# Optimization experiments

Hardware: AMD Instinct MI355X
Metric: run time of the kernel (lower is better)

The kernel has to match this reference:

```python
import jax, jax.numpy as jnp
import numpy as np

B, T, H, OUT_LEN, D_IN, D_OUT = 512, 512, 256, 8, 64, 64

def _lstm_seq(x, Wih, Whh, bih, bhh):
    # batch_first LSTM, zero initial state; x: [B,T,D] -> [B,T,H]
    b = bih + bhh
    h0 = jnp.zeros((x.shape[0], Whh.shape[1]), x.dtype)
    def step(carry, xt):
        h, c = carry
        g = xt @ Wih.T + h @ Whh.T + b
        i, f, gg, o = jnp.split(g, 4, axis=-1)  # torch gate order i,f,g,o
        c = jax.nn.sigmoid(f) * c + jax.nn.sigmoid(i) * jnp.tanh(gg)
        h = jax.nn.sigmoid(o) * jnp.tanh(c)
        return (h, c), h
    _, hs = jax.lax.scan(step, (h0, h0), jnp.swapaxes(x, 0, 1))
    return jnp.swapaxes(hs, 0, 1)

def _lstm_cell0(xt, Wih, bih, bhh):
    # single decode step; original calls self.dec with fresh zero (h,c) each
    # step, so the recurrent matrix Whh never contributes.
    g = xt @ Wih.T + bih + bhh
    i, f, gg, o = jnp.split(g, 4, axis=-1)
    c = jax.nn.sigmoid(i) * jnp.tanh(gg)
    return jax.nn.sigmoid(o) * jnp.tanh(c)

def _mlp(x, Ws, bs, Wl, bl):
    # simple.mlp: hidden Linear+ReLU stack, linear output (dropout off)
    for k in range(Ws.shape[0]):
        x = jax.nn.relu(x @ Ws[k] + bs[k])
    return x @ Wl + bl

def setup_inputs():
    key = jax.random.key(0)
    ks = iter(jax.random.split(key, 32))
    def W(shape, fan):
        return jax.random.normal(next(ks), shape, jnp.float32) / np.float32(np.sqrt(fan))
    return {
        'x': jax.random.normal(next(ks), (B, T, D_IN), jnp.float32),
        'in_W': W((D_IN, H), D_IN), 'in_b': jnp.zeros((H,), jnp.float32),
        'enc_Wih': W((4*H, H), H), 'enc_Whh': W((4*H, H), H),
        'enc_bih': jnp.zeros((4*H,), jnp.float32), 'enc_bhh': jnp.zeros((4*H,), jnp.float32),
        'dec_Wih': W((4*H, 2*H), 2*H), 'dec_Whh': W((4*H, H), H),
        'dec_bih': jnp.zeros((4*H,), jnp.float32), 'dec_bhh': jnp.zeros((4*H,), jnp.float32),
        'w_Ws': W((3, H, H), H), 'w_bs': jnp.zeros((3, H), jnp.float32), 'w_Wl': W((H, H), H), 'w_bl': jnp.zeros((H,), jnp.float32),
        'u_Ws': W((3, H, H), H), 'u_bs': jnp.zeros((3, H), jnp.float32), 'u_Wl': W((H, H), H), 'u_bl': jnp.zeros((H,), jnp.float32),
        'v_Ws': W((7, H, H), H), 'v_bs': jnp.zeros((7, H), jnp.float32), 'v_Wl': W((H, 1), H), 'v_bl': jnp.zeros((1,), jnp.float32),
        'out_W': W((H, D_OUT), H), 'out_b': jnp.zeros((D_OUT,), jnp.float32),
    }

def reference(x, in_W, in_b, enc_Wih, enc_Whh, enc_bih, enc_bhh,
              dec_Wih, dec_Whh, dec_bih, dec_bhh,
              w_Ws, w_bs, w_Wl, w_bl, u_Ws, u_bs, u_Wl, u_bl,
              v_Ws, v_bs, v_Wl, v_bl, out_W, out_b):
    h = x @ in_W + in_b                                       # input projection [B,T,H]
    enc = _lstm_seq(h, enc_Wih, enc_Whh, enc_bih, enc_bhh)    # [B,T,H]
    whs = _mlp(enc, w_Ws, w_bs, w_Wl, w_bl)                   # w(hs), loop-invariant (hoisted)
    def dec_step(s, _):
        us = _mlp(s, u_Ws, u_bs, u_Wl, u_bl)                  # [B,H]
        e = _mlp(jnp.tanh(us[:, None, :] + whs), v_Ws, v_bs, v_Wl, v_bl)  # [B,T,1]
        a = jax.nn.softmax(e, axis=1)                         # softmax over time
        c_t = jnp.sum(a * enc, axis=1)                        # [B,H] weighted sum
        s_new = _lstm_cell0(jnp.concatenate([c_t, s], axis=-1), dec_Wih, dec_bih, dec_bhh)
        return s_new, s_new
    s0 = jnp.zeros((x.shape[0], H), x.dtype)
    _, ss = jax.lax.scan(dec_step, s0, None, length=OUT_LEN)  # [OUT_LEN,B,H]
    dec = jnp.swapaxes(ss, 0, 1)                              # [B,OUT_LEN,H]
    return dec @ out_W + out_b                                # output projection
```

## Files before the change

### kernel.cpp

```cpp
#include <hip/hip_runtime.h>
#include <math.h>

#define B_    512
#define T_    512
#define H_    256
#define DIN_  64
#define OL_   8
#define DOUT_ 64

typedef unsigned short u16;
typedef unsigned int u32;
typedef unsigned long long ull;
typedef __attribute__((ext_vector_type(8))) short short8;
typedef __attribute__((ext_vector_type(4))) float f32x4;

static __device__ __forceinline__ float sigm(float x){ return 1.0f/(1.0f + expf(-x)); }
static __device__ __forceinline__ float bf2f(u16 h){
  u32 u = ((u32)h) << 16; float f; __builtin_memcpy(&f, &u, 4); return f;
}
static __device__ __forceinline__ u16 f2bf(float f){
  u32 u; __builtin_memcpy(&u, &f, 4);
  u = (u + 0x7fffu + ((u >> 16) & 1u)) >> 16;
  return (u16)u;
}
static __device__ __forceinline__ u32 packhl(float f){
  u16 h = f2bf(f);
  u16 lo = f2bf(f - bf2f(h));
  return ((u32)h << 16) | (u32)lo;
}
static __device__ __forceinline__ float unpackhl(u32 w){
  return bf2f((u16)(w >> 16)) + bf2f((u16)(w & 0xffff));
}

__global__ void k_wpt(const float* __restrict__ inW, const float* __restrict__ Wih,
                      float* __restrict__ WpT)
{
  int gid = blockIdx.x * 256 + threadIdx.x;
  int c = gid >> 6, d = gid & 63;
  const float* wr = Wih + c * H_;
  const float* ir = inW + d * H_;
  float acc = 0.f;
  #pragma unroll 4
  for (int e = 0; e < H_; e += 4) {
    float4 av = *(const float4*)(ir + e);
    float4 bv = *(const float4*)(wr + e);
    acc += av.x*bv.x + av.y*bv.y + av.z*bv.z + av.w*bv.w;
  }
  WpT[c*64 + d] = acc;
}

__global__ void k_bp(const float* __restrict__ inb, const float* __restrict__ Wih,
                     const float* __restrict__ bih, const float* __restrict__ bhh,
                     float* __restrict__ bp)
{
  int c = blockIdx.x * 256 + threadIdx.x;
  const float* wr = Wih + c * H_;
  float acc = bih[c] + bhh[c];
  for (int e = 0; e < H_; ++e) acc += inb[e] * wr[e];
  bp[c] = acc;
}

__global__ void k_dwt(const float* __restrict__ dWih, float* __restrict__ dWt)
{
  int gid = blockIdx.x * 256 + threadIdx.x;
  int j = gid >> 9, k = gid & 511;
  int row = (j < 256) ? j : (j + 256);
  dWt[k*768 + j] = dWih[row*512 + k];
}

__global__ void k_wall(const float* __restrict__ wWs, const float* __restrict__ wWl,
                       const float* __restrict__ uWs, const float* __restrict__ uWl,
                       const float* __restrict__ vWs, u16* __restrict__ outb)
{
  int lyr = blockIdx.y;
  const float* W = (lyr < 3)  ? wWs + lyr*65536
                 : (lyr == 3) ? wWl
                 : (lyr < 7)  ? uWs + (lyr-4)*65536
                 : (lyr == 7) ? uWl
                 :              vWs + (lyr-8)*65536;
  u16* out = outb + (size_t)lyr*131072;
  int gid = blockIdx.x * 256 + threadIdx.x;
  int k = gid & 255, n = gid >> 8;
  float v = W[k*256 + n];
  int s = k >> 5, j = k & 7;
  int lane = (((k >> 3) & 3) << 4) | (n & 15);
  int fl = ((s*16) + (n >> 4))*512 + lane*8 + j;
  u16 h = f2bf(v);
  out[fl] = h;
  out[65536 + fl] = f2bf(v - bf2f(h));
}

__global__ void k_whhfl(const float* __restrict__ Whh, u16* __restrict__ out)
{
  int gid = blockIdx.x * 256 + threadIdx.x;
  int j = gid & 7, l = (gid >> 3) & 63, ctg = (gid >> 9) & 63, s = gid >> 15;
  int k = s*32 + (l >> 4)*8 + j;
  int wv = ctg >> 2, g = ctg & 3;
  int row = g*256 + wv*16 + (l & 15);
  float v = Whh[row*256 + k];
  int fl = (s*64 + ctg)*512 + l*8 + j;
  u16 h = f2bf(v);
  out[fl] = h;
  out[262144 + fl] = f2bf(v - bf2f(h));
}

__global__ void k_wpfl(const float* __restrict__ WpT, u16* __restrict__ out)
{
  int gid = blockIdx.x * 256 + threadIdx.x;
  int j = gid & 7, l = (gid >> 3) & 63, ctg = (gid >> 9) & 63, s = gid >> 15;
  int k = s*32 + (l >> 4)*8 + j;
  int wv = ctg >> 2, g = ctg & 3;
  int row = g*256 + wv*16 + (l & 15);
  float v = WpT[row*64 + k];
  int fl = (s*64 + ctg)*512 + l*8 + j;
  u16 h = f2bf(v);
  out[fl] = h;
  out[65536 + fl] = f2bf(v - bf2f(h));
}

__global__ __launch_bounds__(256,1) void k_enc(
    const float* __restrict__ x, const u16* __restrict__ whhFL,
    const u16* __restrict__ wpFL, const float* __restrict__ bp,
    u32* __restrict__ henc, int CB)
{
  __shared__ float G[2][16][32][4];
  const int tid = threadIdx.x, l = tid & 63, wv = tid >> 6;
  const int lr = l & 15, lk = l >> 4;
  const int rg = blockIdx.x, bg = blockIdx.y, z = blockIdx.z;
  const int ug2 = wv >> 1;
  const int g0 = (wv & 1) * 2;
  const int u16g = bg*2 + ug2;

  short8 whH[8][2], whL[8][2], wpH[2][2], wpL[2][2];
  #pragma unroll
  for (int s = 0; s < 8; ++s)
    #pragma unroll
    for (int c = 0; c < 2; ++c) {
      int ctg = u16g*4 + g0 + c;
      whH[s][c] = *(const short8*)(whhFL + ((size_t)(s*64 + ctg))*512 + l*8);
      whL[s][c] = *(const short8*)(whhFL + 262144 + ((size_t)(s*64 + ctg))*512 + l*8);
    }
  #pragma unroll
  for (int s = 0; s < 2; ++s)
    #pragma unroll
    for (int c = 0; c < 2; ++c) {
      int ctg = u16g*4 + g0 + c;
      wpH[s][c] = *(const short8*)(wpFL + ((size_t)(s*64 + ctg))*512 + l*8);
      wpL[s][c] = *(const short8*)(wpFL + 65536 + ((size_t)(s*64 + ctg))*512 + l*8);
    }
  const int ul = tid & 31, er0 = tid >> 5;
  float bb[4];
  #pragma unroll
  for (int g = 0; g < 4; ++g) bb[g] = bp[g*256 + bg*32 + ul];
  float cs[2] = {0.f, 0.f};

  const size_t hstride = (size_t)CB * 256;
  u32* hz = henc + (size_t)z * (size_t)(T_+1) * hstride;
  const float* xrow = x + ((size_t)(z*CB + rg*16 + lr)*T_)*DIN_ + lk*8;

  for (int t = 0; t < T_; ++t) {
    float4 xv0 = *(const float4*)(xrow);
    float4 xv1 = *(const float4*)(xrow + 4);
    float4 xv2 = *(const float4*)(xrow + 32);
    float4 xv3 = *(const float4*)(xrow + 36);
    xrow += DIN_;

    const ull* hb = (const ull*)(hz + (size_t)t*hstride + (size_t)(rg*16 + lr)*256);
    ull hq[8][4];
    #pragma unroll
    for (int s = 0; s < 8; ++s)
      #pragma unroll
      for (int q = 0; q < 4; ++q)
        hq[s][q] = __hip_atomic_load(hb + s*16 + lk*4 + q,
                                     __ATOMIC_RELAXED, __HIP_MEMORY_SCOPE_AGENT);
    if (t) {
      for (;;) {
        bool ok = true;
        #pragma unroll
        for (int s = 0; s < 8; ++s)
          #pragma unroll
          for (int q = 0; q < 4; ++q) {
            u32 a = (u32)hq[s][q], b = (u32)(hq[s][q] >> 32);
            ok = ok && (a != 0u) && (b != 0u);
          }
        if (__all(ok)) break;
        __builtin_amdgcn_s_sleep(1);
        #pragma unroll
        for (int s = 0; s < 8; ++s)
          #pragma unroll
          for (int q = 0; q < 4; ++q)
            hq[s][q] = __hip_atomic_load(hb + s*16 + lk*4 + q,
                                         __ATOMIC_RELAXED, __HIP_MEMORY_SCOPE_AGENT);
      }
    }

    f32x4 acc[2];
    acc[0] = (f32x4){0.f,0.f,0.f,0.f};
    acc[1] = (f32x4){0.f,0.f,0.f,0.f};

    #pragma unroll
    for (int s = 0; s < 2; ++s) {
      float vv[8];
      if (s == 0) { vv[0]=xv0.x;vv[1]=xv0.y;vv[2]=xv0.z;vv[3]=xv0.w;vv[4]=xv1.x;vv[5]=xv1.y;vv[6]=xv1.z;vv[7]=xv1.w; }
      else        { vv[0]=xv2.x;vv[1]=xv2.y;vv[2]=xv2.z;vv[3]=xv2.w;vv[4]=xv3.x;vv[5]=xv3.y;vv[6]=xv3.z;vv[7]=xv3.w; }
      short8 ah, al;
      #pragma unroll
      for (int j = 0; j < 8; ++j) {
        u16 h = f2bf(vv[j]);
        ah[j] = (short)h;
        al[j] = (short)f2bf(vv[j] - bf2f(h));
      }
      #pragma unroll
      for (int c = 0; c < 2; ++c) {
        acc[c] = __builtin_amdgcn_mfma_f32_16x16x32_bf16(ah, wpH[s][c], acc[c], 0,0,0);
        acc[c] = __builtin_amdgcn_mfma_f32_16x16x32_bf16(al, wpH[s][c], acc[c], 0,0,0);
        acc[c] = __builtin_amdgcn_mfma_f32_16x16x32_bf16(ah, wpL[s][c], acc[c], 0,0,0);
      }
    }
    #pragma unroll
    for (int s = 0; s < 8; ++s) {
      short8 ah, al;
      #pragma unroll
      for (int q = 0; q < 4; ++q) {
        u32 w0 = (u32)hq[s][q], w1 = (u32)(hq[s][q] >> 32);
        ah[q*2]   = (short)(w0 >> 16); al[q*2]   = (short)(w0 & 0xffff);
        ah[q*2+1] = (short)(w1 >> 16); al[q*2+1] = (short)(w1 & 0xffff);
      }
      #pragma unroll
      for (int c = 0; c < 2; ++c) {
        acc[c] = __builtin_amdgcn_mfma_f32_16x16x32_bf16(ah, whH[s][c], acc[c], 0,0,0);
        acc[c] = __builtin_amdgcn_mfma_f32_16x16x32_bf16(al, whH[s][c], acc[c], 0,0,0);
        acc[c] = __builtin_amdgcn_mfma_f32_16x16x32_bf16(ah, whL[s][c], acc[c], 0,0,0);
      }
    }

    const int p = t & 1;
    #pragma unroll
    for (int c = 0; c < 2; ++c)
      #pragma unroll
      for (int j = 0; j < 4; ++j)
        G[p][lk*4 + j][ug2*16 + lr][g0 + c] = acc[c][j];
    __syncthreads();

    #pragma unroll
    for (int pp = 0; pp < 2; ++pp) {
      int row = er0 + pp*8;
      float4 gq = *(const float4*)&G[p][row][ul][0];
      float gi = gq.x + bb[0], gf = gq.y + bb[1];
      float gg = gq.z + bb[2], go = gq.w + bb[3];
      float cn = sigm(gf)*cs[pp] + sigm(gi)*tanhf(gg);
      float hn = sigm(go)*tanhf(cn);
      cs[pp] = cn;
      __hip_atomic_store(hz + (size_t)(t+1)*hstride + (size_t)(rg*16 + row)*256 + bg*32 + ul,
                         packhl(hn) | 1u, __ATOMIC_RELAXED, __HIP_MEMORY_SCOPE_AGENT);
    }
  }
}

template<int IN, int FIN, int OUTP>
__global__ __launch_bounds__(256,2) void k_mlp(
    const float* __restrict__ A0, const float* __restrict__ usp,
    const u16* __restrict__ wFL, const float* __restrict__ bs,
    const float* __restrict__ bl, float* __restrict__ Cout,
    float* __restrict__ eout, const float* __restrict__ vWl,
    const float* __restrict__ vbl, int L, int nbs, int cbm1)
{
  extern __shared__ u32 act[];
  const int tid = threadIdx.x, l = tid & 63, cg = tid >> 6;
  const int lr = l & 15, lk = l >> 4;
  const long m0 = (long)blockIdx.x * 64;

  for (int i = tid; i < 4096; i += 256) {
    int row = i >> 6, c16 = i & 63;
    long m = m0 + row;
    uint4 pk;
    if (IN == 2) {
      pk = *(const uint4*)((const u32*)A0 + m*256 + c16*4);
    } else {
      float4 v;
      if (IN == 3) {
        uint4 pw = *(const uint4*)((const u32*)A0 + m*256 + c16*4);
        v.x = unpackhl(pw.x); v.y = unpackhl(pw.y);
        v.z = unpackhl(pw.z); v.w = unpackhl(pw.w);
      } else {
        v = *(const float4*)(A0 + m*256 + c16*4);
      }
      if (IN == 1 || IN == 3) {
        const float* ub = usp + (size_t)(m & cbm1)*256;
        float4 u4 = *(const float4*)(ub + c16*4);
        v.x = tanhf(v.x + u4.x); v.y = tanhf(v.y + u4.y);
        v.z = tanhf(v.z + u4.z); v.w = tanhf(v.w + u4.w);
      }
      pk = (uint4){packhl(v.x), packhl(v.y), packhl(v.z), packhl(v.w)};
    }
    *((uint4*)(act + row*256 + ((c16 ^ (row & 7)) << 2))) = pk;
  }

  f32x4 acc[4][4];
  for (int lyr = 0; lyr < L; ++lyr) {
    __syncthreads();
    const u16* wb = wFL + (size_t)lyr*131072;
    #pragma unroll
    for (int rt = 0; rt < 4; ++rt)
      #pragma unroll
      for (int ct = 0; ct < 4; ++ct) acc[rt][ct] = (f32x4){0.f,0.f,0.f,0.f};

    short8 bh[2][4], blo[2][4];
    #pragma unroll
    for (int ct = 0; ct < 4; ++ct) {
      const u16* bfp = wb + ((size_t)(cg*4 + ct))*512 + l*8;
      bh[0][ct]  = *(const short8*)bfp;
      blo[0][ct] = *(const short8*)(bfp + 65536);
    }
    #pragma unroll
    for (int s = 0; s < 8; ++s) {
      const int pb = s & 1, nb = pb ^ 1;
      if (s < 7) {
        #pragma unroll
        for (int ct = 0; ct < 4; ++ct) {
          const u16* bfp = wb + ((size_t)((s+1)*16 + cg*4 + ct))*512 + l*8;
          bh[nb][ct]  = *(const short8*)bfp;
          blo[nb][ct] = *(const short8*)(bfp + 65536);
        }
      }
      short8 ah[4], al[4];
      #pragma unroll
      for (int rt = 0; rt < 4; ++rt) {
        int row = rt*16 + lr;
        int cc = s*8 + lk*2;
        const u32* base = act + row*256;
        uint4 d0 = *(const uint4*)(base + (((cc    ) ^ (row & 7)) << 2));
        uint4 d1 = *(const uint4*)(base + (((cc + 1) ^ (row & 7)) << 2));
        u32 q[8] = {d0.x,d0.y,d0.z,d0.w,d1.x,d1.y,d1.z,d1.w};
        #pragma unroll
        for (int j = 0; j < 8; ++j) {
          ah[rt][j] = (short)(q[j] >> 16);
          al[rt][j] = (short)(q[j] & 0xffff);
        }
      }
      #pragma unroll
      for (int ct = 0; ct < 4; ++ct)
        #pragma unroll
        for (int rt = 0; rt < 4; ++rt) {
          acc[rt][ct] = __builtin_amdgcn_mfma_f32_16x16x32_bf16(ah[rt], bh[pb][ct],  acc[rt][ct], 0,0,0);
          acc[rt][ct] = __builtin_amdgcn_mfma_f32_16x16x32_bf16(al[rt], bh[pb][ct],  acc[rt][ct], 0,0,0);
          acc[rt][ct] = __builtin_amdgcn_mfma_f32_16x16x32_bf16(ah[rt], blo[pb][ct], acc[rt][ct], 0,0,0);
        }
    }
    const float* bptr = (lyr < nbs) ? (bs + lyr*256) : bl;
    const bool dorelu = (lyr < L-1) || (FIN == 1);
    #pragma unroll
    for (int ct = 0; ct < 4; ++ct) {
      float bv = bptr[cg*64 + ct*16 + lr];
      #pragma unroll
      for (int rt = 0; rt < 4; ++rt)
        #pragma unroll
        for (int g = 0; g < 4; ++g) {
          float xv = acc[rt][ct][g] + bv;
          acc[rt][ct][g] = dorelu ? fmaxf(xv, 0.f) : xv;
        }
    }
    if (lyr == L-1) break;
    __syncthreads();
    #pragma unroll
    for (int ct = 0; ct < 4; ++ct) {
      int n = cg*64 + ct*16 + lr;
      #pragma unroll
      for (int rt = 0; rt < 4; ++rt)
        #pragma unroll
        for (int g = 0; g < 4; ++g) {
          int row = rt*16 + lk*4 + g;
          act[row*256 + (((n >> 2) ^ (row & 7)) << 2) + (n & 3)] = packhl(acc[rt][ct][g]);
        }
    }
  }

  if (FIN == 0) {
    #pragma unroll
    for (int ct = 0; ct < 4; ++ct) {
      int n = cg*64 + ct*16 + lr;
      #pragma unroll
      for (int rt = 0; rt < 4; ++rt)
        #pragma unroll
        for (int g = 0; g < 4; ++g) {
          long m = m0 + rt*16 + lk*4 + g;
          if (OUTP) ((u32*)Cout)[m*256 + n] = packhl(acc[rt][ct][g]);
          else      Cout[m*256 + n] = acc[rt][ct][g];
        }
    }
  } else {
    float part[4][4];
    #pragma unroll
    for (int rt = 0; rt < 4; ++rt)
      #pragma unroll
      for (int g = 0; g < 4; ++g) part[rt][g] = 0.f;
    #pragma unroll
    for (int ct = 0; ct < 4; ++ct) {
      float vw = vWl[cg*64 + ct*16 + lr];
      #pragma unroll
      for (int rt = 0; rt < 4; ++rt)
        #pragma unroll
        for (int g = 0; g < 4; ++g) part[rt][g] += acc[rt][ct][g] * vw;
    }
    #pragma unroll
    for (int o = 1; o < 16; o <<= 1)
      #pragma unroll
      for (int rt = 0; rt < 4; ++rt)
        #pragma unroll
        for (int g = 0; g < 4; ++g) part[rt][g] += __shfl_xor(part[rt][g], o, 64);
    __syncthreads();
    float* ep = (float*)act;
    if ((l & 15) == 0) {
      #pragma unroll
      for (int rt = 0; rt < 4; ++rt)
        #pragma unroll
        for (int g = 0; g < 4; ++g)
          ep[cg*64 + rt*16 + lk*4 + g] = part[rt][g];
    }
    __syncthreads();
    if (tid < 64)
      eout[m0 + tid] = ep[tid] + ep[64 + tid] + ep[128 + tid] + ep[192 + tid] + vbl[0];
  }
}

__global__ __launch_bounds__(256,2) void k_attn(const float* __restrict__ e,
    const u32* __restrict__ henc, float* __restrict__ ct, int CB)
{
  __shared__ float as[512];
  __shared__ float red[8];
  const int b = blockIdx.x, tid = threadIdx.x;
  const int lane = tid & 63, w = tid >> 6;
  float v0 = e[(size_t)tid*CB + b];
  float v1 = e[(size_t)(tid + 256)*CB + b];
  float m = fmaxf(v0, v1);
  #pragma unroll
  for (int o = 32; o; o >>= 1) m = fmaxf(m, __shfl_xor(m, o, 64));
  if (!lane) red[w] = m;
  __syncthreads();
  m = fmaxf(fmaxf(red[0], red[1]), fmaxf(red[2], red[3]));
  float x0 = expf(v0 - m), x1 = expf(v1 - m);
  float sm = x0 + x1;
  #pragma unroll
  for (int o = 32; o; o >>= 1) sm += __shfl_xor(sm, o, 64);
  if (!lane) red[4 + w] = sm;
  __syncthreads();
  float inv = 1.f / (red[4] + red[5] + red[6] + red[7]);
  as[tid] = x0 * inv;
  as[256 + tid] = x1 * inv;
  __syncthreads();
  float acc = 0.f;
  const u32* ep = henc + (size_t)(CB + b)*256 + tid;
  const size_t ts = (size_t)CB * 256;
  #pragma unroll 8
  for (int t = 0; t < 512; ++t) acc += as[t] * unpackhl(ep[t*ts]);
  ct[b*H_ + tid] = acc;
}

__global__ __launch_bounds__(256,2) void k_dec_cell(
    const float* __restrict__ ct, float* __restrict__ s, const float* __restrict__ dWt,
    const float* __restrict__ bih, const float* __restrict__ bhh,
    float* __restrict__ dec, int step)
{
  __shared__ float xt[4][516];
  const int tid = threadIdx.x;
  const int b0 = blockIdx.x * 4;
  for (int f = tid; f < 4*128; f += 256) {
    int bb = f >> 7, k4 = f & 127;
    float4 v = (k4 < 64) ? *(const float4*)(ct + (b0+bb)*H_ + k4*4)
                         : *(const float4*)(s  + (b0+bb)*H_ + (k4-64)*4);
    *(float4*)(&xt[bb][k4*4]) = v;
  }
  __syncthreads();
  const int u = tid;
  float ai[4], ag[4], ao[4];
  #pragma unroll
  for (int bb = 0; bb < 4; ++bb) { ai[bb]=0.f; ag[bb]=0.f; ao[bb]=0.f; }
  #pragma unroll 4
  for (int k = 0; k < 512; ++k) {
    float wi = dWt[k*768 + u];
    float wg = dWt[k*768 + 256 + u];
    float wo = dWt[k*768 + 512 + u];
    #pragma unroll
    for (int bb = 0; bb < 4; ++bb) {
      float xv = xt[bb][k];
      ai[bb] += xv*wi; ag[bb] += xv*wg; ao[bb] += xv*wo;
    }
  }
  float bi = bih[u]       + bhh[u];
  float bg = bih[512 + u] + bhh[512 + u];
  float bo = bih[768 + u] + bhh[768 + u];
  #pragma unroll
  for (int bb = 0; bb < 4; ++bb) {
    int b = b0 + bb;
    float cn = sigm(ai[bb] + bi) * tanhf(ag[bb] + bg);
    float hn = sigm(ao[bb] + bo) * tanhf(cn);
    s[b*H_ + u] = hn;
    dec[((size_t)b*OL_ + step)*H_ + u] = hn;
  }
}

__global__ __launch_bounds__(256,2) void k_outproj(
    const float* __restrict__ dec, const float* __restrict__ oW,
    const float* __restrict__ ob, float* __restrict__ out)
{
  const int tid = threadIdx.x;
  const int m0 = blockIdx.x * 16;
  const int d = tid & 63, rr = tid >> 6;
  float bv = ob[d];
  for (int p = 0; p < 4; ++p) {
    int m = m0 + p*4 + rr;
    const float* ar = dec + (size_t)m*H_;
    float acc = bv;
    #pragma unroll 4
    for (int k = 0; k < H_; ++k) acc += ar[k] * oW[k*64 + d];
    out[(size_t)m*64 + d] = acc;
  }
}

extern "C" void kernel_launch(void* const* d_in, const int* in_sizes, int n_in,
                              void* d_out, int out_size, void* d_ws, size_t ws_size,
                              hipStream_t stream)
{
  (void)in_sizes; (void)n_in;
  const float* x    = (const float*)d_in[0];
  const float* inW  = (const float*)d_in[1];
  const float* inb  = (const float*)d_in[2];
  const float* eWih = (const float*)d_in[3];
  const float* eWhh = (const float*)d_in[4];
  const float* ebih = (const float*)d_in[5];
  const float* ebhh = (const float*)d_in[6];
  const float* dWih = (const float*)d_in[7];
  const float* dbih = (const float*)d_in[9];
  const float* dbhh = (const float*)d_in[10];
  const float* wWs  = (const float*)d_in[11];
  const float* wbs  = (const float*)d_in[12];
  const float* wWl  = (const float*)d_in[13];
  const float* wbl  = (const float*)d_in[14];
  const float* uWs  = (const float*)d_in[15];
  const float* ubs  = (const float*)d_in[16];
  const float* uWl  = (const float*)d_in[17];
  const float* ubl  = (const float*)d_in[18];
  const float* vWs  = (const float*)d_in[19];
  const float* vbs  = (const float*)d_in[20];
  const float* vWl  = (const float*)d_in[21];
  const float* vbl  = (const float*)d_in[22];
  const float* oW   = (const float*)d_in[23];
  const float* ob   = (const float*)d_in[24];
  float* out = (float*)d_out;

  hipFuncSetAttribute((const void*)k_mlp<0,0,0>, hipFuncAttributeMaxDynamicSharedMemorySize, 65536);
  hipFuncSetAttribute((const void*)k_mlp<2,0,1>, hipFuncAttributeMaxDynamicSharedMemorySize, 65536);
  hipFuncSetAttribute((const void*)k_mlp<3,1,0>, hipFuncAttributeMaxDynamicSharedMemorySize, 65536);

  const int CB = 128;
  const size_t hsz = (size_t)(T_+1)*CB*256;
  const size_t avail = ws_size / 4;
  auto need = [&](int nc) -> size_t {
    return (size_t)nc*hsz
         + (size_t)CB*T_*256/1
         - (size_t)CB*T_*256 + (size_t)CB*T_*256
         + (size_t)CB*3328 + 1300000ull;
  };
  auto needf = [&](int nc) -> size_t {
    return (size_t)nc*hsz + (size_t)CB*T_*256 + (size_t)CB*3328 + 1300000ull;
  };
  (void)need;
  int NC = (needf(2) <= avail) ? 2 : 1;
  if (needf(NC) > avail) { hipMemsetAsync(d_out, 0, (size_t)out_size*4, stream); return; }

  float* wsf = (float*)d_ws;
  size_t o = 0;
  u32* henc = (u32*)(wsf + o);  o += (size_t)NC*hsz;
  u32* whsP = (u32*)(wsf + o);  o += (size_t)CB*T_*256;
  float* sbuf= wsf + o;  o += (size_t)CB*256;
  float* us  = wsf + o;  o += (size_t)CB*256;
  float* ctx = wsf + o;  o += (size_t)CB*256;
  float* dec = wsf + o;  o += (size_t)CB*2048;
  float* e   = wsf + o;  o += (size_t)CB*512;
  float* WpT = wsf + o;  o += 65536;
  float* bp  = wsf + o;  o += 1024;
  float* dWt = wsf + o;  o += 393216;
  u16* whhFL = (u16*)(wsf + o);  o += 262144;
  u16* wpFL  = (u16*)(wsf + o);  o += 65536;
  u16* mlpFL = (u16*)(wsf + o);

  k_wpt<<<256, 256, 0, stream>>>(inW, eWih, WpT);
  k_bp <<<4,   256, 0, stream>>>(inb, eWih, ebih, ebhh, bp);
  k_dwt<<<1536,256, 0, stream>>>(dWih, dWt);
  k_whhfl<<<1024,256,0,stream>>>(eWhh, whhFL);
  k_wpfl <<<256, 256,0,stream>>>(WpT, wpFL);
  k_wall <<<dim3(256,15), 256, 0, stream>>>(wWs, wWl, uWs, uWl, vWs, mlpFL);

  const int gBig = CB * 8;
  const int gU   = CB / 64;
  const int cbm1 = CB - 1;

  for (int c0 = 0; c0 < B_; c0 += CB*NC) {
    hipMemsetAsync(henc, 0, (size_t)NC*hsz*4, stream);

    k_enc<<<dim3(CB/16, 8, NC), 256, 0, stream>>>(
        x + (size_t)c0*T_*DIN_, whhFL, wpFL, bp, henc, CB);

    for (int z = 0; z < NC; ++z) {
      int c = c0 + z*CB;
      u32* hz = henc + (size_t)z*hsz;
      float* outc = out + (size_t)c*OL_*DOUT_;

      hipMemsetAsync(sbuf, 0, (size_t)CB*1024, stream);

      k_mlp<2,0,1><<<gBig, 256, 65536, stream>>>((const float*)(hz + (size_t)CB*256),
                                                 nullptr, mlpFL, wbs, wbl,
                                                 (float*)whsP, nullptr, nullptr, nullptr, 4, 3, 0);

      for (int step = 0; step < OL_; ++step) {
        k_mlp<0,0,0><<<gU, 256, 65536, stream>>>(sbuf, nullptr, mlpFL + 4ull*131072, ubs, ubl,
                                                 us, nullptr, nullptr, nullptr, 4, 3, 0);
        k_mlp<3,1,0><<<gBig, 256, 65536, stream>>>((const float*)whsP, us, mlpFL + 8ull*131072,
                                                   vbs, nullptr, nullptr, e, vWl, vbl, 7, 7, cbm1);
        k_attn<<<CB, 256, 0, stream>>>(e, hz, ctx, CB);
        k_dec_cell<<<CB/4, 256, 0, stream>>>(ctx, sbuf, dWt, dbih, dbhh, dec, step);
      }
      k_outproj<<<CB/2, 256, 0, stream>>>(dec, oW, ob, outc);
    }
  }
}
```

Baseline: 19.20 ms.

## Fuse decoder stages into one persistent kernel with flag-based inter-block sync

```diff
diff --git a/kernel.cpp b/kernel.cpp
--- a/kernel.cpp
+++ b/kernel.cpp
@@ -8,6 +8,9 @@
 #define OL_   8
 #define DOUT_ 64
 
+#define CBv   128
+#define HSTR  32768
+
 typedef unsigned short u16;
 typedef unsigned int u32;
 typedef unsigned long long ull;
@@ -30,6 +33,12 @@
 }
 static __device__ __forceinline__ float unpackhl(u32 w){
   return bf2f((u16)(w >> 16)) + bf2f((u16)(w & 0xffff));
+}
+static __device__ __forceinline__ u32 al(const u32* p){
+  return __hip_atomic_load(p, __ATOMIC_RELAXED, __HIP_MEMORY_SCOPE_AGENT);
+}
+static __device__ __forceinline__ void as_(u32* p, u32 v){
+  __hip_atomic_store(p, v, __ATOMIC_RELAXED, __HIP_MEMORY_SCOPE_AGENT);
 }
 
 __global__ void k_wpt(const float* __restrict__ inW, const float* __restrict__ Wih,
@@ -121,7 +130,7 @@
 __global__ __launch_bounds__(256,1) void k_enc(
     const float* __restrict__ x, const u16* __restrict__ whhFL,
     const u16* __restrict__ wpFL, const float* __restrict__ bp,
-    u32* __restrict__ henc, int CB)
+    u32* __restrict__ henc)
 {
   __shared__ float G[2][16][32][4];
   const int tid = threadIdx.x, l = tid & 63, wv = tid >> 6;
@@ -154,9 +163,8 @@
   for (int g = 0; g < 4; ++g) bb[g] = bp[g*256 + bg*32 + ul];
   float cs[2] = {0.f, 0.f};
 
-  const size_t hstride = (size_t)CB * 256;
-  u32* hz = henc + (size_t)z * (size_t)(T_+1) * hstride;
-  const float* xrow = x + ((size_t)(z*CB + rg*16 + lr)*T_)*DIN_ + lk*8;
+  u32* hz = henc + (size_t)z * (size_t)(T_+1) * HSTR;
+  const float* xrow = x + ((size_t)(z*CBv + rg*16 + lr)*T_)*DIN_ + lk*8;
 
   for (int t = 0; t < T_; ++t) {
     float4 xv0 = *(const float4*)(xrow);
@@ -165,7 +173,7 @@
     float4 xv3 = *(const float4*)(xrow + 36);
     xrow += DIN_;
 
-    const ull* hb = (const ull*)(hz + (size_t)t*hstride + (size_t)(rg*16 + lr)*256);
+    const ull* hb = (const ull*)(hz + (size_t)t*HSTR + (size_t)(rg*16 + lr)*256);
     ull hq[8][4];
     #pragma unroll
     for (int s = 0; s < 8; ++s)
@@ -203,34 +211,34 @@
       float vv[8];
       if (s == 0) { vv[0]=xv0.x;vv[1]=xv0.y;vv[2]=xv0.z;vv[3]=xv0.w;vv[4]=xv1.x;vv[5]=xv1.y;vv[6]=xv1.z;vv[7]=xv1.w; }
       else        { vv[0]=xv2.x;vv[1]=xv2.y;vv[2]=xv2.z;vv[3]=xv2.w;vv[4]=xv3.x;vv[5]=xv3.y;vv[6]=xv3.z;vv[7]=xv3.w; }
-      short8 ah, al;
+      short8 ah, al2;
       #pragma unroll
       for (int j = 0; j < 8; ++j) {
         u16 h = f2bf(vv[j]);
         ah[j] = (short)h;
-        al[j] = (short)f2bf(vv[j] - bf2f(h));
+        al2[j] = (short)f2bf(vv[j] - bf2f(h));
       }
       #pragma unroll
       for (int c = 0; c < 2; ++c) {
-        acc[c] = __builtin_amdgcn_mfma_f32_16x16x32_bf16(ah, wpH[s][c], acc[c], 0,0,0);
-        acc[c] = __builtin_amdgcn_mfma_f32_16x16x32_bf16(al, wpH[s][c], acc[c], 0,0,0);
-        acc[c] = __builtin_amdgcn_mfma_f32_16x16x32_bf16(ah, wpL[s][c], acc[c], 0,0,0);
+        acc[c] = __builtin_amdgcn_mfma_f32_16x16x32_bf16(ah,  wpH[s][c], acc[c], 0,0,0);
+        acc[c] = __builtin_amdgcn_mfma_f32_16x16x32_bf16(al2, wpH[s][c], acc[c], 0,0,0);
+        acc[c] = __builtin_amdgcn_mfma_f32_16x16x32_bf16(ah,  wpL[s][c], acc[c], 0,0,0);
       }
     }
     #pragma unroll
     for (int s = 0; s < 8; ++s) {
-      short8 ah, al;
+      short8 ah, al2;
       #pragma unroll
       for (int q = 0; q < 4; ++q) {
         u32 w0 = (u32)hq[s][q], w1 = (u32)(hq[s][q] >> 32);
-        ah[q*2]   = (short)(w0 >> 16); al[q*2]   = (short)(w0 & 0xffff);
-        ah[q*2+1] = (short)(w1 >> 16); al[q*2+1] = (short)(w1 & 0xffff);
+        ah[q*2]   = (short)(w0 >> 16); al2[q*2]   = (short)(w0 & 0xffff);
+        ah[q*2+1] = (short)(w1 >> 16); al2[q*2+1] = (short)(w1 & 0xffff);
       }
       #pragma unroll
       for (int c = 0; c < 2; ++c) {
-        acc[c] = __builtin_amdgcn_mfma_f32_16x16x32_bf16(ah, whH[s][c], acc[c], 0,0,0);
-        acc[c] = __builtin_amdgcn_mfma_f32_16x16x32_bf16(al, whH[s][c], acc[c], 0,0,0);
-        acc[c] = __builtin_amdgcn_mfma_f32_16x16x32_bf16(ah, whL[s][c], acc[c], 0,0,0);
+        acc[c] = __builtin_amdgcn_mfma_f32_16x16x32_bf16(ah,  whH[s][c], acc[c], 0,0,0);
+        acc[c] = __builtin_amdgcn_mfma_f32_16x16x32_bf16(al2, whH[s][c], acc[c], 0,0,0);
+        acc[c] = __builtin_amdgcn_mfma_f32_16x16x32_bf16(ah,  whL[s][c], acc[c], 0,0,0);
       }
     }
 
@@ -251,51 +259,18 @@
       float cn = sigm(gf)*cs[pp] + sigm(gi)*tanhf(gg);
       float hn = sigm(go)*tanhf(cn);
       cs[pp] = cn;
-      __hip_atomic_store(hz + (size_t)(t+1)*hstride + (size_t)(rg*16 + row)*256 + bg*32 + ul,
-                         packhl(hn) | 1u, __ATOMIC_RELAXED, __HIP_MEMORY_SCOPE_AGENT);
+      as_(hz + (size_t)(t+1)*HSTR + (size_t)(rg*16 + row)*256 + bg*32 + ul,
+          packhl(hn) | 1u);
     }
   }
 }
 
-template<int IN, int FIN, int OUTP>
-__global__ __launch_bounds__(256,2) void k_mlp(
-    const float* __restrict__ A0, const float* __restrict__ usp,
-    const u16* __restrict__ wFL, const float* __restrict__ bs,
-    const float* __restrict__ bl, float* __restrict__ Cout,
-    float* __restrict__ eout, const float* __restrict__ vWl,
-    const float* __restrict__ vbl, int L, int nbs, int cbm1)
-{
-  extern __shared__ u32 act[];
-  const int tid = threadIdx.x, l = tid & 63, cg = tid >> 6;
+static __device__ __forceinline__ void mlp_core(
+    u32* act, const u16* wFL, const float* bs, const float* bl,
+    int L, int nbs, bool lastRelu, int tid)
+{
+  const int l = tid & 63, cg = tid >> 6;
   const int lr = l & 15, lk = l >> 4;
-  const long m0 = (long)blockIdx.x * 64;
-
-  for (int i = tid; i < 4096; i += 256) {
-    int row = i >> 6, c16 = i & 63;
-    long m = m0 + row;
-    uint4 pk;
-    if (IN == 2) {
-      pk = *(const uint4*)((const u32*)A0 + m*256 + c16*4);
-    } else {
-      float4 v;
-      if (IN == 3) {
-        uint4 pw = *(const uint4*)((const u32*)A0 + m*256 + c16*4);
-        v.x = unpackhl(pw.x); v.y = unpackhl(pw.y);
-        v.z = unpackhl(pw.z); v.w = unpackhl(pw.w);
-      } else {
-        v = *(const float4*)(A0 + m*256 + c16*4);
-      }
-      if (IN == 1 || IN == 3) {
-        const float* ub = usp + (size_t)(m & cbm1)*256;
-        float4 u4 = *(const float4*)(ub + c16*4);
-        v.x = tanhf(v.x + u4.x); v.y = tanhf(v.y + u4.y);
-        v.z = tanhf(v.z + u4.z); v.w = tanhf(v.w + u4.w);
-      }
-      pk = (uint4){packhl(v.x), packhl(v.y), packhl(v.z), packhl(v.w)};
-    }
-    *((uint4*)(act + row*256 + ((c16 ^ (row & 7)) << 2))) = pk;
-  }
-
   f32x4 acc[4][4];
   for (int lyr = 0; lyr < L; ++lyr) {
     __syncthreads();
@@ -323,7 +298,7 @@
           blo[nb][ct] = *(const short8*)(bfp + 65536);
         }
       }
-      short8 ah[4], al[4];
+      short8 ah[4], al2[4];
       #pragma unroll
       for (int rt = 0; rt < 4; ++rt) {
         int row = rt*16 + lr;
@@ -334,21 +309,21 @@
         u32 q[8] = {d0.x,d0.y,d0.z,d0.w,d1.x,d1.y,d1.z,d1.w};
         #pragma unroll
         for (int j = 0; j < 8; ++j) {
-          ah[rt][j] = (short)(q[j] >> 16);
-          al[rt][j] = (short)(q[j] & 0xffff);
+          ah[rt][j]  = (short)(q[j] >> 16);
+          al2[rt][j] = (short)(q[j] & 0xffff);
         }
       }
       #pragma unroll
       for (int ct = 0; ct < 4; ++ct)
         #pragma unroll
         for (int rt = 0; rt < 4; ++rt) {
-          acc[rt][ct] = __builtin_amdgcn_mfma_f32_16x16x32_bf16(ah[rt], bh[pb][ct],  acc[rt][ct], 0,0,0);
-          acc[rt][ct] = __builtin_amdgcn_mfma_f32_16x16x32_bf16(al[rt], bh[pb][ct],  acc[rt][ct], 0,0,0);
-          acc[rt][ct] = __builtin_amdgcn_mfma_f32_16x16x32_bf16(ah[rt], blo[pb][ct], acc[rt][ct], 0,0,0);
+          acc[rt][ct] = __builtin_amdgcn_mfma_f32_16x16x32_bf16(ah[rt],  bh[pb][ct],  acc[rt][ct], 0,0,0);
+          acc[rt][ct] = __builtin_amdgcn_mfma_f32_16x16x32_bf16(al2[rt], bh[pb][ct],  acc[rt][ct], 0,0,0);
+          acc[rt][ct] = __builtin_amdgcn_mfma_f32_16x16x32_bf16(ah[rt],  blo[pb][ct], acc[rt][ct], 0,0,0);
         }
     }
     const float* bptr = (lyr < nbs) ? (bs + lyr*256) : bl;
-    const bool dorelu = (lyr < L-1) || (FIN == 1);
+    const bool dorelu = (lyr < L-1) || lastRelu;
     #pragma unroll
     for (int ct = 0; ct < 4; ++ct) {
       float bv = bptr[cg*64 + ct*16 + lr];
@@ -360,7 +335,6 @@
           acc[rt][ct][g] = dorelu ? fmaxf(xv, 0.f) : xv;
         }
     }
-    if (lyr == L-1) break;
     __syncthreads();
     #pragma unroll
     for (int ct = 0; ct < 4; ++ct) {
@@ -374,146 +348,216 @@
         }
     }
   }
-
-  if (FIN == 0) {
-    #pragma unroll
-    for (int ct = 0; ct < 4; ++ct) {
-      int n = cg*64 + ct*16 + lr;
-      #pragma unroll
-      for (int rt = 0; rt < 4; ++rt)
-        #pragma unroll
-        for (int g = 0; g < 4; ++g) {
-          long m = m0 + rt*16 + lk*4 + g;
-          if (OUTP) ((u32*)Cout)[m*256 + n] = packhl(acc[rt][ct][g]);
-          else      Cout[m*256 + n] = acc[rt][ct][g];
-        }
-    }
-  } else {
-    float part[4][4];
-    #pragma unroll
-    for (int rt = 0; rt < 4; ++rt)
-      #pragma unroll
-      for (int g = 0; g < 4; ++g) part[rt][g] = 0.f;
-    #pragma unroll
-    for (int ct = 0; ct < 4; ++ct) {
-      float vw = vWl[cg*64 + ct*16 + lr];
-      #pragma unroll
-      for (int rt = 0; rt < 4; ++rt)
-        #pragma unroll
-        for (int g = 0; g < 4; ++g) part[rt][g] += acc[rt][ct][g] * vw;
-    }
-    #pragma unroll
-    for (int o = 1; o < 16; o <<= 1)
-      #pragma unroll
-      for (int rt = 0; rt < 4; ++rt)
-        #pragma unroll
-        for (int g = 0; g < 4; ++g) part[rt][g] += __shfl_xor(part[rt][g], o, 64);
+  __syncthreads();
+}
+
+__global__ __launch_bounds__(256,1) void k_dec_all(
+    const u32* __restrict__ henc, const u16* __restrict__ mlpFL,
+    const float* __restrict__ wbs, const float* __restrict__ wbl,
+    const float* __restrict__ ubs, const float* __restrict__ ubl,
+    const float* __restrict__ vbs, const float* __restrict__ vWl,
+    const float* __restrict__ vbl,
+    const float* __restrict__ dWt, const float* __restrict__ dbih,
+    const float* __restrict__ dbhh,
+    const float* __restrict__ oW, const float* __restrict__ ob,
+    u32* __restrict__ whsP, u32* __restrict__ usb, u32* __restrict__ usflag,
+    u32* __restrict__ eS, u32* __restrict__ ctxS, u32* __restrict__ sS,
+    float* __restrict__ outc)
+{
+  extern __shared__ u32 act[];
+  __shared__ float red[8];
+  const int bid = blockIdx.x, tid = threadIdx.x;
+  const u16* wFLw = mlpFL;
+  const u16* wFLu = mlpFL + 4*131072;
+  const u16* wFLv = mlpFL + 8*131072;
+  float sprev[4] = {0.f, 0.f, 0.f, 0.f};
+
+  for (int k = 0; k < 4; ++k) {
+    long m0t = (long)(bid + 256*k) * 64;
     __syncthreads();
-    float* ep = (float*)act;
-    if ((l & 15) == 0) {
-      #pragma unroll
-      for (int rt = 0; rt < 4; ++rt)
-        #pragma unroll
-        for (int g = 0; g < 4; ++g)
-          ep[cg*64 + rt*16 + lk*4 + g] = part[rt][g];
-    }
-    __syncthreads();
-    if (tid < 64)
-      eout[m0 + tid] = ep[tid] + ep[64 + tid] + ep[128 + tid] + ep[192 + tid] + vbl[0];
+    for (int i = tid; i < 4096; i += 256) {
+      int row = i >> 6, c16 = i & 63;
+      long m = m0t + row;
+      uint4 pk = *(const uint4*)(henc + HSTR + m*256 + c16*4);
+      *((uint4*)(act + row*256 + ((c16 ^ (row & 7)) << 2))) = pk;
+    }
+    mlp_core(act, wFLw, wbs, wbl, 4, 3, false, tid);
+    for (int i = tid; i < 4096; i += 256) {
+      int row = i >> 6, c16 = i & 63;
+      long m = m0t + row;
+      uint4 pk = *((const uint4*)(act + row*256 + ((c16 ^ (row & 7)) << 2)));
+      *(uint4*)(whsP + m*256 + c16*4) = pk;
+    }
   }
-}
-
-__global__ __launch_bounds__(256,2) void k_attn(const float* __restrict__ e,
-    const u32* __restrict__ henc, float* __restrict__ ct, int CB)
-{
-  __shared__ float as[512];
-  __shared__ float red[8];
-  const int b = blockIdx.x, tid = threadIdx.x;
-  const int lane = tid & 63, w = tid >> 6;
-  float v0 = e[(size_t)tid*CB + b];
-  float v1 = e[(size_t)(tid + 256)*CB + b];
-  float m = fmaxf(v0, v1);
-  #pragma unroll
-  for (int o = 32; o; o >>= 1) m = fmaxf(m, __shfl_xor(m, o, 64));
-  if (!lane) red[w] = m;
-  __syncthreads();
-  m = fmaxf(fmaxf(red[0], red[1]), fmaxf(red[2], red[3]));
-  float x0 = expf(v0 - m), x1 = expf(v1 - m);
-  float sm = x0 + x1;
-  #pragma unroll
-  for (int o = 32; o; o >>= 1) sm += __shfl_xor(sm, o, 64);
-  if (!lane) red[4 + w] = sm;
-  __syncthreads();
-  float inv = 1.f / (red[4] + red[5] + red[6] + red[7]);
-  as[tid] = x0 * inv;
-  as[256 + tid] = x1 * inv;
-  __syncthreads();
-  float acc = 0.f;
-  const u32* ep = henc + (size_t)(CB + b)*256 + tid;
-  const size_t ts = (size_t)CB * 256;
-  #pragma unroll 8
-  for (int t = 0; t < 512; ++t) acc += as[t] * unpackhl(ep[t*ts]);
-  ct[b*H_ + tid] = acc;
-}
-
-__global__ __launch_bounds__(256,2) void k_dec_cell(
-    const float* __restrict__ ct, float* __restrict__ s, const float* __restrict__ dWt,
-    const float* __restrict__ bih, const float* __restrict__ bhh,
-    float* __restrict__ dec, int step)
-{
-  __shared__ float xt[4][516];
-  const int tid = threadIdx.x;
-  const int b0 = blockIdx.x * 4;
-  for (int f = tid; f < 4*128; f += 256) {
-    int bb = f >> 7, k4 = f & 127;
-    float4 v = (k4 < 64) ? *(const float4*)(ct + (b0+bb)*H_ + k4*4)
-                         : *(const float4*)(s  + (b0+bb)*H_ + (k4-64)*4);
-    *(float4*)(&xt[bb][k4*4]) = v;
-  }
-  __syncthreads();
-  const int u = tid;
-  float ai[4], ag[4], ao[4];
-  #pragma unroll
-  for (int bb = 0; bb < 4; ++bb) { ai[bb]=0.f; ag[bb]=0.f; ao[bb]=0.f; }
-  #pragma unroll 4
-  for (int k = 0; k < 512; ++k) {
-    float wi = dWt[k*768 + u];
-    float wg = dWt[k*768 + 256 + u];
-    float wo = dWt[k*768 + 512 + u];
-    #pragma unroll
-    for (int bb = 0; bb < 4; ++bb) {
-      float xv = xt[bb][k];
-      ai[bb] += xv*wi; ag[bb] += xv*wg; ao[bb] += xv*wo;
-    }
-  }
-  float bi = bih[u]       + bhh[u];
-  float bg = bih[512 + u] + bhh[512 + u];
-  float bo = bih[768 + u] + bhh[768 + u];
-  #pragma unroll
-  for (int bb = 0; bb < 4; ++bb) {
-    int b = b0 + bb;
-    float cn = sigm(ai[bb] + bi) * tanhf(ag[bb] + bg);
-    float hn = sigm(ao[bb] + bo) * tanhf(cn);
-    s[b*H_ + u] = hn;
-    dec[((size_t)b*OL_ + step)*H_ + u] = hn;
-  }
-}
-
-__global__ __launch_bounds__(256,2) void k_outproj(
-    const float* __restrict__ dec, const float* __restrict__ oW,
-    const float* __restrict__ ob, float* __restrict__ out)
-{
-  const int tid = threadIdx.x;
-  const int m0 = blockIdx.x * 16;
-  const int d = tid & 63, rr = tid >> 6;
-  float bv = ob[d];
-  for (int p = 0; p < 4; ++p) {
-    int m = m0 + p*4 + rr;
-    const float* ar = dec + (size_t)m*H_;
-    float acc = bv;
-    #pragma unroll 4
-    for (int k = 0; k < H_; ++k) acc += ar[k] * oW[k*64 + d];
-    out[(size_t)m*64 + d] = acc;
+
+  for (int s = 0; s < OL_; ++s) {
+    if (bid < 2) {
+      long m0t = (long)bid * 64;
+      __syncthreads();
+      for (int i = tid; i < 4096; i += 256) {
+        int row = i >> 6, c16 = i & 63;
+        const u32* sp = sS + (size_t)s*32768 + (m0t + row)*256 + c16*4;
+        u32 w0 = al(sp), w1 = al(sp+1), w2 = al(sp+2), w3 = al(sp+3);
+        if (s) {
+          while (!(w0 && w1 && w2 && w3)) {
+            __builtin_amdgcn_s_sleep(1);
+            w0 = al(sp); w1 = al(sp+1); w2 = al(sp+2); w3 = al(sp+3);
+          }
+        }
+        uint4 pk = { packhl(__uint_as_float(w0)), packhl(__uint_as_float(w1)),
+                     packhl(__uint_as_float(w2)), packhl(__uint_as_float(w3)) };
+        *((uint4*)(act + row*256 + ((c16 ^ (row & 7)) << 2))) = pk;
+      }
+      mlp_core(act, wFLu, ubs, ubl, 4, 3, false, tid);
+      for (int i = tid; i < 4096; i += 256) {
+        int row = i >> 6, c16 = i & 63;
+        uint4 pk = *((const uint4*)(act + row*256 + ((c16 ^ (row & 7)) << 2)));
+        *(uint4*)(usb + (size_t)s*32768 + (m0t + row)*256 + c16*4) = pk;
+      }
+      __syncthreads();
+      if (tid == 0)
+        __hip_atomic_store(usflag + s*2 + bid, 1u,
+                           __ATOMIC_RELEASE, __HIP_MEMORY_SCOPE_AGENT);
+    }
+
+    {
+      const u32* f0 = usflag + s*2;
+      for (;;) {
+        u32 a0 = al(f0), a1 = al(f0 + 1);
+        if (a0 & a1) break;
+        __builtin_amdgcn_s_sleep(2);
+      }
+      __builtin_amdgcn_fence(__ATOMIC_ACQUIRE, "agent");
+    }
+
+    for (int k = 0; k < 4; ++k) {
+      long m0t = (long)(bid + 256*k) * 64;
+      __syncthreads();
+      for (int i = tid; i < 4096; i += 256) {
+        int row = i >> 6, c16 = i & 63;
+        long m = m0t + row;
+        uint4 pw = *(const uint4*)(whsP + m*256 + c16*4);
+        uint4 uw = *(const uint4*)(usb + (size_t)s*32768 + (m & 127)*256 + c16*4);
+        uint4 pk;
+        pk.x = packhl(tanhf(unpackhl(pw.x) + unpackhl(uw.x)));
+        pk.y = packhl(tanhf(unpackhl(pw.y) + unpackhl(uw.y)));
+        pk.z = packhl(tanhf(unpackhl(pw.z) + unpackhl(uw.z)));
+        pk.w = packhl(tanhf(unpackhl(pw.w) + unpackhl(uw.w)));
+        *((uint4*)(act + row*256 + ((c16 ^ (row & 7)) << 2))) = pk;
+      }
+      mlp_core(act, wFLv, vbs, vbs, 7, 7, true, tid);
+      {
+        int r2 = tid >> 2, q = tid & 3;
+        float p = 0.f;
+        #pragma unroll 8
+        for (int j = 0; j < 64; ++j) {
+          int n = q*64 + j;
+          u32 w = act[r2*256 + (((n >> 2) ^ (r2 & 7)) << 2) + (n & 3)];
+          p += unpackhl(w) * vWl[n];
+        }
+        p += __shfl_xor(p, 1, 64);
+        p += __shfl_xor(p, 2, 64);
+        if (q == 0)
+          as_(eS + (size_t)s*65536 + m0t + r2, __float_as_uint(p + vbl[0]) | 1u);
+      }
+    }
+
+    if (bid >= 64 && bid < 192) {
+      int b = bid - 64;
+      __syncthreads();
+      float* asx = (float*)act;
+      const u32* ep0 = eS + (size_t)s*65536 + b;
+      u32 w0, w1;
+      for (;;) {
+        w0 = al(ep0 + (size_t)tid*128);
+        w1 = al(ep0 + (size_t)(tid + 256)*128);
+        if (w0 && w1) break;
+        __builtin_amdgcn_s_sleep(1);
+      }
+      float v0 = __uint_as_float(w0), v1 = __uint_as_float(w1);
+      const int lane = tid & 63, wv = tid >> 6;
+      float m = fmaxf(v0, v1);
+      #pragma unroll
+      for (int o = 32; o; o >>= 1) m = fmaxf(m, __shfl_xor(m, o, 64));
+      if (!lane) red[wv] = m;
+      __syncthreads();
+      m = fmaxf(fmaxf(red[0], red[1]), fmaxf(red[2], red[3]));
+      float x0 = expf(v0 - m), x1 = expf(v1 - m);
+      float sm = x0 + x1;
+      #pragma unroll
+      for (int o = 32; o; o >>= 1) sm += __shfl_xor(sm, o, 64);
+      if (!lane) red[4 + wv] = sm;
+      __syncthreads();
+      float inv = 1.f / (red[4] + red[5] + red[6] + red[7]);
+      asx[tid] = x0 * inv;
+      asx[256 + tid] = x1 * inv;
+      __syncthreads();
+      float accv = 0.f;
+      const u32* hp = henc + HSTR + (size_t)b*256 + tid;
+      #pragma unroll 8
+      for (int t = 0; t < 512; ++t) accv += asx[t] * unpackhl(hp[(size_t)t*HSTR]);
+      as_(ctxS + (size_t)s*32768 + b*256 + tid, __float_as_uint(accv) | 1u);
+    }
+
+    if (bid >= 224) {
+      int c = bid - 224, b0r = c*4;
+      __syncthreads();
+      float* xt = (float*)act;
+      float cv[4];
+      {
+        const u32* cp = ctxS + (size_t)s*32768 + (size_t)b0r*256 + tid;
+        u32 w0, w1, w2, w3;
+        for (;;) {
+          w0 = al(cp); w1 = al(cp + 256); w2 = al(cp + 512); w3 = al(cp + 768);
+          if (w0 && w1 && w2 && w3) break;
+          __builtin_amdgcn_s_sleep(1);
+        }
+        cv[0] = __uint_as_float(w0); cv[1] = __uint_as_float(w1);
+        cv[2] = __uint_as_float(w2); cv[3] = __uint_as_float(w3);
+      }
+      #pragma unroll
+      for (int bb = 0; bb < 4; ++bb) {
+        xt[bb*520 + tid] = cv[bb];
+        xt[bb*520 + 256 + tid] = sprev[bb];
+      }
+      __syncthreads();
+      float ai[4], ag[4], ao[4];
+      #pragma unroll
+      for (int bb = 0; bb < 4; ++bb) { ai[bb]=0.f; ag[bb]=0.f; ao[bb]=0.f; }
+      #pragma unroll 4
+      for (int k = 0; k < 512; ++k) {
+        float wi = dWt[k*768 + tid];
+        float wg = dWt[k*768 + 256 + tid];
+        float wo = dWt[k*768 + 512 + tid];
+        #pragma unroll
+        for (int bb = 0; bb < 4; ++bb) {
+          float xv = xt[bb*520 + k];
+          ai[bb] += xv*wi; ag[bb] += xv*wg; ao[bb] += xv*wo;
+        }
+      }
+      float bi = dbih[tid]       + dbhh[tid];
+      float bg = dbih[512 + tid] + dbhh[512 + tid];
+      float bo = dbih[768 + tid] + dbhh[768 + tid];
+      float snew[4];
+      #pragma unroll
+      for (int bb = 0; bb < 4; ++bb) {
+        float cn = sigm(ai[bb] + bi) * tanhf(ag[bb] + bg);
+        snew[bb] = sigm(ao[bb] + bo) * tanhf(cn);
+        as_(sS + (size_t)(s+1)*32768 + (size_t)(b0r + bb)*256 + tid,
+            __float_as_uint(snew[bb]) | 1u);
+        sprev[bb] = snew[bb];
+      }
+      __syncthreads();
+      float* sn = (float*)act;
+      #pragma unroll
+      for (int bb = 0; bb < 4; ++bb) sn[bb*256 + tid] = snew[bb];
+      __syncthreads();
+      int d = tid & 63, rr = tid >> 6;
+      float a2 = ob[d];
+      #pragma unroll 4
+      for (int k = 0; k < 256; ++k) a2 += sn[rr*256 + k] * oW[k*64 + d];
+      outc[((size_t)(b0r + rr)*OL_ + s)*64 + d] = a2;
+    }
   }
 }
 
@@ -548,35 +592,26 @@
   const float* ob   = (const float*)d_in[24];
   float* out = (float*)d_out;
 
-  hipFuncSetAttribute((const void*)k_mlp<0,0,0>, hipFuncAttributeMaxDynamicSharedMemorySize, 65536);
-  hipFuncSetAttribute((const void*)k_mlp<2,0,1>, hipFuncAttributeMaxDynamicSharedMemorySize, 65536);
-  hipFuncSetAttribute((const void*)k_mlp<3,1,0>, hipFuncAttributeMaxDynamicSharedMemorySize, 65536);
-
-  const int CB = 128;
-  const size_t hsz = (size_t)(T_+1)*CB*256;
+  hipFuncSetAttribute((const void*)k_dec_all, hipFuncAttributeMaxDynamicSharedMemorySize, 65536);
+
+  const size_t hsz = (size_t)(T_+1) * HSTR;
   const size_t avail = ws_size / 4;
-  auto need = [&](int nc) -> size_t {
-    return (size_t)nc*hsz
-         + (size_t)CB*T_*256/1
-         - (size_t)CB*T_*256 + (size_t)CB*T_*256
-         + (size_t)CB*3328 + 1300000ull;
+  auto needf = [&](int nc) -> size_t {
+    return (size_t)nc*hsz + 16777216ull  + 1343552ull
+         + 1770496ull  + 4096;
   };
-  auto needf = [&](int nc) -> size_t {
-    return (size_t)nc*hsz + (size_t)CB*T_*256 + (size_t)CB*3328 + 1300000ull;
-  };
-  (void)need;
   int NC = (needf(2) <= avail) ? 2 : 1;
   if (needf(NC) > avail) { hipMemsetAsync(d_out, 0, (size_t)out_size*4, stream); return; }
 
   float* wsf = (float*)d_ws;
   size_t o = 0;
   u32* henc = (u32*)(wsf + o);  o += (size_t)NC*hsz;
-  u32* whsP = (u32*)(wsf + o);  o += (size_t)CB*T_*256;
-  float* sbuf= wsf + o;  o += (size_t)CB*256;
-  float* us  = wsf + o;  o += (size_t)CB*256;
-  float* ctx = wsf + o;  o += (size_t)CB*256;
-  float* dec = wsf + o;  o += (size_t)CB*2048;
-  float* e   = wsf + o;  o += (size_t)CB*512;
+  u32* whsP = (u32*)(wsf + o);  o += 16777216;
+  u32* usb  = (u32*)(wsf + o);  o += 262144;
+  u32* usflag = (u32*)(wsf + o); o += 64;
+  u32* eS   = (u32*)(wsf + o);  o += 524288;
+  u32* ctxS = (u32*)(wsf + o);  o += 262144;
+  u32* sS   = (u32*)(wsf + o);  o += 294912;
   float* WpT = wsf + o;  o += 65536;
   float* bp  = wsf + o;  o += 1024;
   float* dWt = wsf + o;  o += 393216;
@@ -584,6 +619,8 @@
   u16* wpFL  = (u16*)(wsf + o);  o += 65536;
   u16* mlpFL = (u16*)(wsf + o);
 
+  const size_t scratchBytes = (262144ull + 64 + 524288 + 262144 + 294912) * 4;
+
   k_wpt<<<256, 256, 0, stream>>>(inW, eWih, WpT);
   k_bp <<<4,   256, 0, stream>>>(inb, eWih, ebih, ebhh, bp);
   k_dwt<<<1536,256, 0, stream>>>(dWih, dWt);
@@ -591,36 +628,20 @@
   k_wpfl <<<256, 256,0,stream>>>(WpT, wpFL);
   k_wall <<<dim3(256,15), 256, 0, stream>>>(wWs, wWl, uWs, uWl, vWs, mlpFL);
 
-  const int gBig = CB * 8;
-  const int gU   = CB / 64;
-  const int cbm1 = CB - 1;
-
-  for (int c0 = 0; c0 < B_; c0 += CB*NC) {
+  for (int c0 = 0; c0 < B_; c0 += CBv*NC) {
     hipMemsetAsync(henc, 0, (size_t)NC*hsz*4, stream);
 
-    k_enc<<<dim3(CB/16, 8, NC), 256, 0, stream>>>(
-        x + (size_t)c0*T_*DIN_, whhFL, wpFL, bp, henc, CB);
+    k_enc<<<dim3(CBv/16, 8, NC), 256, 0, stream>>>(
+        x + (size_t)c0*T_*DIN_, whhFL, wpFL, bp, henc);
 
     for (int z = 0; z < NC; ++z) {
-      int c = c0 + z*CB;
-      u32* hz = henc + (size_t)z*hsz;
-      float* outc = out + (size_t)c*OL_*DOUT_;
-
-      hipMemsetAsync(sbuf, 0, (size_t)CB*1024, stream);
-
-      k_mlp<2,0,1><<<gBig, 256, 65536, stream>>>((const float*)(hz + (size_t)CB*256),
-                                                 nullptr, mlpFL, wbs, wbl,
-                                                 (float*)whsP, nullptr, nullptr, nullptr, 4, 3, 0);
-
-      for (int step = 0; step < OL_; ++step) {
-        k_mlp<0,0,0><<<gU, 256, 65536, stream>>>(sbuf, nullptr, mlpFL + 4ull*131072, ubs, ubl,
-                                                 us, nullptr, nullptr, nullptr, 4, 3, 0);
-        k_mlp<3,1,0><<<gBig, 256, 65536, stream>>>((const float*)whsP, us, mlpFL + 8ull*131072,
-                                                   vbs, nullptr, nullptr, e, vWl, vbl, 7, 7, cbm1);
-        k_attn<<<CB, 256, 0, stream>>>(e, hz, ctx, CB);
-        k_dec_cell<<<CB/4, 256, 0, stream>>>(ctx, sbuf, dWt, dbih, dbhh, dec, step);
-      }
-      k_outproj<<<CB/2, 256, 0, stream>>>(dec, oW, ob, outc);
+      hipMemsetAsync(usb, 0, scratchBytes, stream);
+      k_dec_all<<<256, 256, 65536, stream>>>(
+          henc + (size_t)z*hsz, mlpFL,
+          wbs, wbl, ubs, ubl, vbs, vWl, vbl,
+          dWt, dbih, dbhh, oW, ob,
+          whsP, usb, usflag, eS, ctxS, sS,
+          out + (size_t)(c0 + z*CBv)*OL_*DOUT_);
     }
   }
 }
```

Result: faster. 18.68 ms (-2.7%).
